# Kernel tuning notes

Hardware: AMD Instinct MI355X
Metric: run time of the kernel (lower is better)

## Reference

```python
import jax, jax.numpy as jnp
import numpy as np

B, T, TM = 4, 1024, 1500
D_MODEL, D_FFN, H, D_HEAD, D_MEM = 1024, 4096, 16, 64, 1024
EPS = 1e-5


def layernorm(x, g):
    m = jnp.mean(x, axis=-1, keepdims=True)
    xc = x - m
    v = jnp.mean(xc * xc, axis=-1, keepdims=True)
    return xc * jax.lax.rsqrt(v + EPS) * g


def setup_inputs() -> dict:
    key = jax.random.key(0)
    ks = jax.random.split(key, 12)
    s = lambda fan_in: 1.0 / np.sqrt(fan_in)
    return {
        "x": jax.random.normal(ks[0], (B, T, D_MODEL), jnp.float32),
        "encoder_output": jax.random.normal(ks[1], (B, TM, D_MEM), jnp.float32),
        "encoder_mask": jax.random.randint(ks[2], (B, TM), 0, 2).astype(bool),
        "w_qkv": jax.random.normal(ks[3], (D_MODEL, 3 * H * D_HEAD), jnp.float32) * s(D_MODEL),
        "w_o_sa": jax.random.normal(ks[4], (H * D_HEAD, D_MODEL), jnp.float32) * s(H * D_HEAD),
        "w_q": jax.random.normal(ks[5], (D_MODEL, H * D_HEAD), jnp.float32) * s(D_MODEL),
        "w_kv": jax.random.normal(ks[6], (D_MEM, 2 * H * D_HEAD), jnp.float32) * s(D_MEM),
        "w_o_xa": jax.random.normal(ks[7], (H * D_HEAD, D_MODEL), jnp.float32) * s(H * D_HEAD),
        "w_ff1": jax.random.normal(ks[8], (D_MODEL, D_FFN), jnp.float32) * s(D_MODEL),
        "w_ff2": jax.random.normal(ks[9], (D_FFN, D_MODEL), jnp.float32) * s(D_FFN),
        "g_sa": jnp.ones((D_MODEL,), jnp.float32),
        "g_xaq": jnp.ones((D_MODEL,), jnp.float32),
        "g_xam": jnp.ones((D_MEM,), jnp.float32),
        "g_ff": jnp.ones((D_MODEL,), jnp.float32),
    }


def reference(x, encoder_output, encoder_mask, w_qkv, w_o_sa, w_q, w_kv, w_o_xa,
              w_ff1, w_ff2, g_sa, g_xaq, g_xam, g_ff):
    b, t, _ = x.shape
    scale = D_HEAD ** -0.5

    # ---- causal self-attention ----
    residual = x
    xn = layernorm(x, g_sa)
    qkv = (xn @ w_qkv).reshape(b, t, 3, H, D_HEAD)
    q, k, v = qkv[:, :, 0], qkv[:, :, 1], qkv[:, :, 2]  # (B,T,H,D)
    scores = jnp.einsum('bqhd,bkhd->bhqk', q, k) * scale
    causal = jnp.tril(jnp.ones((t, t), x.dtype))
    scores = scores + (1.0 - causal) * -1e9
    attn = jax.nn.softmax(scores, axis=-1)
    sa = jnp.einsum('bhqk,bkhd->bqhd', attn, v).reshape(b, t, H * D_HEAD)
    x = residual + sa @ w_o_sa

    # ---- cross-attention ----
    residual = x
    qn = layernorm(x, g_xaq)
    mn = layernorm(encoder_output, g_xam)
    tq, tm = t, mn.shape[1]
    qx = (qn @ w_q).reshape(b, tq, H, D_HEAD)
    kvx = (mn @ w_kv).reshape(b, tm, 2, H, D_HEAD)
    kx, vx = kvx[:, :, 0], kvx[:, :, 1]
    xs = jnp.einsum('bqhd,bkhd->bhqk', qx, kx) * scale
    xs = jnp.where(encoder_mask[:, None, None, :], xs, -jnp.inf)
    xattn = jax.nn.softmax(xs, axis=-1)
    xa = jnp.einsum('bhqk,bkhd->bqhd', xattn, vx).reshape(b, tq, H * D_HEAD)
    x = residual + xa @ w_o_xa

    # ---- pointwise FFN (kernel_size=1 conv == linear) ----
    residual = x
    h = layernorm(x, g_ff)
    h = jax.nn.gelu(h @ w_ff1, approximate=True) @ w_ff2
    x = residual + h
    return (x, k, v)
```

## Files before the change

### kernel.cpp

```cpp
#include <hip/hip_runtime.h>
#include <hip/hip_bf16.h>
#include <cstdint>
#include <cstddef>


typedef __attribute__((ext_vector_type(4))) float f32x4;
typedef __attribute__((ext_vector_type(8))) short s8v;
typedef __attribute__((ext_vector_type(2))) unsigned uint2v;

#define DEVI __device__ __forceinline__

DEVI short f2bf(float f) {
  union { float f; unsigned u; } x; x.f = f;
  unsigned r = x.u + 0x7fffu + ((x.u >> 16) & 1u);
  return (short)(r >> 16);
}
DEVI float bf2f(short s) {
  union { unsigned u; float f; } x; x.u = ((unsigned)(unsigned short)s) << 16;
  return x.f;
}
DEVI unsigned cvtpk_bf2(float lo, float hi) {
  unsigned r;
  asm("v_cvt_pk_bf16_f32 %0, %1, %2" : "=v"(r) : "v"(lo), "v"(hi));
  return r;
}
DEVI float fexp2(float x) {
  float r;
  asm("v_exp_f32 %0, %1" : "=v"(r) : "v"(x));
  return r;
}
DEVI float bpermf(int srclane, float v) {
  union { float f; int i; } x; x.f = v;
  x.i = __builtin_amdgcn_ds_bpermute(srclane << 2, x.i);
  return x.f;
}
DEVI void gload_lds16(const void* g, void* l) {
  __builtin_amdgcn_global_load_lds((const __attribute__((address_space(1))) void*)g,
                                   (__attribute__((address_space(3))) void*)l,
                                   16, 0, 0);
}

__global__ __launch_bounds__(256) void k_transpose_cvt(
    const float* __restrict__ w, short* __restrict__ wt, int K, int N) {
  __shared__ float tile[32][33];
  int n0 = blockIdx.x * 32, k0 = blockIdx.y * 32;
  int tx = threadIdx.x & 31, ty = threadIdx.x >> 5;
#pragma unroll
  for (int i = 0; i < 32; i += 8)
    tile[ty + i][tx] = w[(size_t)(k0 + ty + i) * N + n0 + tx];
  __syncthreads();
#pragma unroll
  for (int i = 0; i < 32; i += 8)
    wt[(size_t)(n0 + ty + i) * K + k0 + tx] = f2bf(tile[tx][ty + i]);
}

__global__ __launch_bounds__(256) void k_vtrans(
    const short* __restrict__ src, int srs, int coff,
    short* __restrict__ dst, int T, int Tp) {
  __shared__ short tile[32][72];
  int bh = blockIdx.y, b = bh >> 4, h = bh & 15;
  int t0 = blockIdx.x * 32;
  const short* sB = src + (size_t)b * T * srs + coff + h * 64;
  short* dB = dst + (size_t)bh * 64 * Tp;
  int t = threadIdx.x;
  int r = t >> 3, c = (t & 7) * 8;
  int tr = t0 + r; if (tr > T - 1) tr = T - 1;
  *(s8v*)&tile[r][c] = *(const s8v*)(sB + (size_t)tr * srs + c);
  __syncthreads();
  int d = t & 63, ch = t >> 6;
  s8v o;
#pragma unroll
  for (int j = 0; j < 8; j++) o[j] = tile[ch * 8 + j][d];
  *(s8v*)(dB + (size_t)d * Tp + t0 + ch * 8) = o;
}

__global__ void k_maskpack(const int* __restrict__ mask,
                           unsigned long long* __restrict__ out, int Tk, int mw) {
  int b = blockIdx.x, w = threadIdx.x;
  if (w >= mw) return;
  unsigned long long v = 0;
  const int* mb = mask + (size_t)b * Tk;
#pragma unroll 4
  for (int j = 0; j < 64; j++) {
    int k = w * 64 + j;
    if (k < Tk && mb[k]) v |= (1ull << j);
  }
  out[(size_t)b * mw + w] = v;
}

__global__ __launch_bounds__(256) void k_ln(
    const float* __restrict__ x, const float* __restrict__ g,
    short* __restrict__ out) {
  int row = blockIdx.x;
  const float* xr = x + (size_t)row * 1024;
  int t = threadIdx.x, wid = t >> 6, lane = t & 63;
  f32x4 v = ((const f32x4*)xr)[t];
  float s = v[0] + v[1] + v[2] + v[3];
#pragma unroll
  for (int m = 32; m >= 1; m >>= 1) s += __shfl_xor(s, m);
  __shared__ float red[4];
  if (lane == 0) red[wid] = s;
  __syncthreads();
  float mean = (red[0] + red[1] + red[2] + red[3]) * (1.f / 1024.f);
  float q = 0.f;
#pragma unroll
  for (int i = 0; i < 4; i++) { v[i] -= mean; q += v[i] * v[i]; }
#pragma unroll
  for (int m = 32; m >= 1; m >>= 1) q += __shfl_xor(q, m);
  __syncthreads();
  if (lane == 0) red[wid] = q;
  __syncthreads();
  float var = (red[0] + red[1] + red[2] + red[3]) * (1.f / 1024.f);
  float rs = rsqrtf(var + 1e-5f);
  f32x4 gv = ((const f32x4*)g)[t];
  unsigned w0 = cvtpk_bf2(v[0] * rs * gv[0], v[1] * rs * gv[1]);
  unsigned w1 = cvtpk_bf2(v[2] * rs * gv[2], v[3] * rs * gv[3]);
  uint2v w = {w0, w1};
  *(uint2v*)(out + (size_t)row * 1024 + t * 4) = w;
}

template <bool RES, bool GELU_, bool F32OUT, bool BF16OUT>
__global__ __launch_bounds__(256) void k_gemm(
    const short* __restrict__ A, const short* __restrict__ Bt,
    float* __restrict__ Cf, short* __restrict__ Cb,
    const float* __restrict__ res, int M, int N, int K, int lda, int ldb) {
  __shared__ short As[128 * 64];
  __shared__ short Bs[128 * 64];
  int z = blockIdx.z;
  A += (size_t)z * K;
  Bt += (size_t)z * K;
  if (F32OUT) Cf += (size_t)z * M * N;
  int t = threadIdx.x, wid = t >> 6, lane = t & 63;
  int la = lane & 15, lb = lane >> 4;
  int wr = wid >> 1, wc = wid & 1;
  int am = blockIdx.x * 128, bn = blockIdx.y * 128;

  f32x4 acc[4][4];
#pragma unroll
  for (int m = 0; m < 4; m++)
#pragma unroll
    for (int n = 0; n < 4; n++) acc[m][n] = (f32x4){0.f, 0.f, 0.f, 0.f};

  for (int k0 = 0; k0 < K; k0 += 64) {
#pragma unroll
    for (int i = 0; i < 4; i++) {
      int fl = i * 256 + t;
      int r = fl >> 3;
      int c = ((fl & 7) ^ (r & 7)) << 3;
      int ar = am + r; if (ar > M - 1) ar = M - 1;
      gload_lds16(A + (size_t)ar * lda + k0 + c, As + (size_t)(i * 256 + wid * 64) * 8);
      int br = bn + r;
      gload_lds16(Bt + (size_t)br * ldb + k0 + c, Bs + (size_t)(i * 256 + wid * 64) * 8);
    }
    __syncthreads();
#pragma unroll
    for (int kk = 0; kk < 2; kk++) {
      s8v af[4], bfg[4];
#pragma unroll
      for (int m = 0; m < 4; m++)
        af[m] = *(const s8v*)(As + (wr * 64 + m * 16 + la) * 64 +
                              ((kk * 32 + lb * 8) ^ ((la & 7) << 3)));
#pragma unroll
      for (int n = 0; n < 4; n++)
        bfg[n] = *(const s8v*)(Bs + (wc * 64 + n * 16 + la) * 64 +
                               ((kk * 32 + lb * 8) ^ ((la & 7) << 3)));
#pragma unroll
      for (int m = 0; m < 4; m++)
#pragma unroll
        for (int n = 0; n < 4; n++)
          acc[m][n] = __builtin_amdgcn_mfma_f32_16x16x32_bf16(af[m], bfg[n], acc[m][n], 0, 0, 0);
    }
    __syncthreads();
  }

#pragma unroll
  for (int m = 0; m < 4; m++) {
    int rb = am + wr * 64 + m * 16 + lb * 4;
#pragma unroll
    for (int n = 0; n < 4; n++) {
      int col = bn + wc * 64 + n * 16 + la;
#pragma unroll
      for (int j = 0; j < 4; j++) {
        int r = rb + j;
        if (r < M) {
          float v = acc[m][n][j];
          if (RES) v += res[(size_t)r * N + col];
          if (GELU_) {
            float u = v;
            float y = 0.7978845608f * u * (1.f + 0.044715f * u * u);
            float e = fexp2(fminf(y * 2.88539008f, 80.f));
            float th = (e - 1.f) * __builtin_amdgcn_rcpf(e + 1.f);
            v = 0.5f * u * (1.f + th);
          }
          if (F32OUT) Cf[(size_t)r * N + col] = v;
          if (BF16OUT) Cb[(size_t)r * N + col] = f2bf(v);
        }
      }
    }
  }
}

__global__ __launch_bounds__(256) void k_red4(
    const f32x4* __restrict__ p, const f32x4* __restrict__ res,
    f32x4* __restrict__ out, int n) {
  size_t i = (size_t)blockIdx.x * 256 + threadIdx.x;
  f32x4 v = res[i] + (p[i] + p[i + (size_t)n]) +
            (p[i + 2 * (size_t)n] + p[i + 3 * (size_t)n]);
  out[i] = v;
}

template <bool CAUSAL>
__global__ __launch_bounds__(512) void k_attn4(
    const short* __restrict__ qbuf, int qrs,
    const short* __restrict__ kbuf, int krs,
    const short* __restrict__ vT, int vts,
    short* __restrict__ obuf, int ors,
    const unsigned long long* __restrict__ mbits, int mwords,
    int Tq, int Tk, float scale) {
  __shared__ short Ks[64 * 64];
  __shared__ short Vs[64 * 64];
  __shared__ short Ps[8 * 1024];
  int bh = blockIdx.y, b = bh >> 4, h = bh & 15;
  int t = threadIdx.x, wid = t >> 6, lane = t & 63;
  int la = lane & 15, lb = lane >> 4;
  float lscale = scale * 1.44269504f;

  const short* qB = qbuf + (size_t)b * Tq * qrs + h * 64;
  const short* kB = kbuf + (size_t)b * Tk * krs + h * 64;
  const short* vB = vT + (size_t)bh * 64 * vts;
  char* Pw = (char*)(Ps + wid * 1024);

  int sr = t >> 3, scol = (t & 7) * 8;
  int swz = sr * 64 + (scol ^ ((sr & 7) << 3));

  int nsup = CAUSAL ? 2 : 1;
  for (int s = 0; s < nsup; s++) {
    int st = CAUSAL ? (s ? 7 - blockIdx.x : blockIdx.x) : blockIdx.x;
    int q0 = st * 128 + wid * 16;
    int nkt = CAUSAL ? 2 * st + 2 : (Tk + 63) >> 6;
    int lastkt = CAUSAL ? (q0 >> 6) : nkt - 1;

    s8v qf[2];
#pragma unroll
    for (int kk = 0; kk < 2; kk++)
      qf[kk] = *(const s8v*)(qB + (size_t)(q0 + la) * qrs + kk * 32 + lb * 8);

    f32x4 accO[4];
#pragma unroll
    for (int n = 0; n < 4; n++) accO[n] = (f32x4){0.f, 0.f, 0.f, 0.f};
    float m = -1e30f, l = 0.f;

    s8v krg, vrg;
    {
      int tk = sr; if (tk > Tk - 1) tk = Tk - 1;
      krg = *(const s8v*)(kB + (size_t)tk * krs + scol);
      vrg = *(const s8v*)(vB + (size_t)sr * vts + scol);
    }

    for (int kt = 0; kt < nkt; kt++) {
      int kb0 = kt << 6;
      __syncthreads();
      *(s8v*)&Ks[swz] = krg;
      *(s8v*)&Vs[swz] = vrg;
      __syncthreads();
      if (kt + 1 < nkt) {
        int kb = kb0 + 64;
        int tk = kb + sr; if (tk > Tk - 1) tk = Tk - 1;
        krg = *(const s8v*)(kB + (size_t)tk * krs + scol);
        vrg = *(const s8v*)(vB + (size_t)sr * vts + kb + scol);
      }
      if (kt > lastkt) continue;

      bool needMask;
      unsigned long long wm = ~0ull;
      if (CAUSAL) {
        needMask = (kt == lastkt);
      } else {
        wm = mbits[(size_t)b * mwords + kt];
        needMask = (wm != ~0ull);
      }

      float sc[4][4];
      __builtin_amdgcn_s_setprio(1);
#pragma unroll
      for (int n = 0; n < 4; n++) {
        f32x4 a = (f32x4){0.f, 0.f, 0.f, 0.f};
#pragma unroll
        for (int kk = 0; kk < 2; kk++) {
          s8v kf = *(const s8v*)&Ks[(n * 16 + la) * 64 +
                                    ((kk * 32 + lb * 8) ^ ((la & 7) << 3))];
          a = __builtin_amdgcn_mfma_f32_16x16x32_bf16(kf, qf[kk], a, 0, 0, 0);
        }
#pragma unroll
        for (int j = 0; j < 4; j++) {
          float sv = a[j] * lscale;
          if (needMask) {
            int ki = n * 16 + lb * 4 + j;
            bool ok = CAUSAL ? (kb0 + ki <= q0 + la) : (((wm >> ki) & 1ull) != 0);
            sv = ok ? sv : -1e30f;
          }
          sc[n][j] = sv;
        }
      }
      __builtin_amdgcn_s_setprio(0);

      float tm = sc[0][0];
#pragma unroll
      for (int n = 0; n < 4; n++)
#pragma unroll
        for (int j = 0; j < 4; j++) tm = fmaxf(tm, sc[n][j]);
      tm = fmaxf(tm, __shfl_xor(tm, 16));
      tm = fmaxf(tm, __shfl_xor(tm, 32));
      tm = fmaxf(tm, -1e4f);

      bool skip = __all(tm - m <= 10.f);
      float alpha = 1.f;
      if (!skip) {
        float mn_ = fmaxf(m, tm);
        alpha = fexp2(m - mn_);
        m = mn_;
      }

      unsigned W[4][2];
      float ps = 0.f;
#pragma unroll
      for (int n = 0; n < 4; n++) {
        float p0 = fexp2(sc[n][0] - m), p1 = fexp2(sc[n][1] - m);
        float p2 = fexp2(sc[n][2] - m), p3 = fexp2(sc[n][3] - m);
        ps += (p0 + p1) + (p2 + p3);
        W[n][0] = cvtpk_bf2(p0, p1);
        W[n][1] = cvtpk_bf2(p2, p3);
      }
      ps += __shfl_xor(ps, 16);
      ps += __shfl_xor(ps, 32);
      l = l * alpha + ps;

      if (!skip) {
#pragma unroll
        for (int j = 0; j < 4; j++) {
          float aj = bpermf(lb * 20 + j, alpha);
#pragma unroll
          for (int n = 0; n < 4; n++) accO[n][j] *= aj;
        }
      }

#pragma unroll
      for (int n = 0; n < 4; n++) {
        uint2v w2 = {W[n][0], W[n][1]};
        *(uint2v*)(Pw + ((la * 128 + n * 32 + lb * 8) ^ ((la & 7) << 4))) = w2;
      }
      __builtin_amdgcn_s_setprio(1);
#pragma unroll
      for (int kk = 0; kk < 2; kk++) {
        s8v pa = *(const s8v*)(Pw + ((la * 128 + kk * 64 + lb * 16) ^ ((la & 7) << 4)));
#pragma unroll
        for (int n = 0; n < 4; n++) {
          s8v vf = *(const s8v*)&Vs[(n * 16 + la) * 64 +
                                    ((kk * 32 + lb * 8) ^ ((la & 7) << 3))];
          accO[n] = __builtin_amdgcn_mfma_f32_16x16x32_bf16(pa, vf, accO[n], 0, 0, 0);
        }
      }
      __builtin_amdgcn_s_setprio(0);
    }

#pragma unroll
    for (int j = 0; j < 4; j++) {
      float lj = bpermf(lb * 20 + j, l);
      float inv = 1.f / lj;
      int r = q0 + lb * 4 + j;
#pragma unroll
      for (int n = 0; n < 4; n++)
        obuf[(size_t)(b * Tq + r) * ors + h * 64 + n * 16 + la] = f2bf(accO[n][j] * inv);
    }
  }
}

__global__ __launch_bounds__(256) void k_copy_kv(
    const short* __restrict__ qkvb, float* __restrict__ ok, float* __restrict__ ov) {
  size_t i = (size_t)blockIdx.x * 256 + threadIdx.x;
  size_t row = i >> 7, c8 = (i & 127) << 3;
  const short* base = qkvb + row * 3072;
  s8v kv = *(const s8v*)(base + 1024 + c8);
  s8v vv = *(const s8v*)(base + 2048 + c8);
  f32x4 k0, k1, v0, v1;
#pragma unroll
  for (int j = 0; j < 4; j++) {
    k0[j] = bf2f(kv[j]); k1[j] = bf2f(kv[4 + j]);
    v0[j] = bf2f(vv[j]); v1[j] = bf2f(vv[4 + j]);
  }
  float* okp = ok + row * 1024 + c8;
  float* ovp = ov + row * 1024 + c8;
  *(f32x4*)okp = k0; *(f32x4*)(okp + 4) = k1;
  *(f32x4*)ovp = v0; *(f32x4*)(ovp + 4) = v1;
}

extern "C" void kernel_launch(void* const* d_in, const int* in_sizes, int n_in,
                              void* d_out, int out_size, void* d_ws, size_t ws_size,
                              hipStream_t stream) {
  (void)in_sizes; (void)n_in; (void)out_size; (void)ws_size;
  const float* x      = (const float*)d_in[0];
  const float* enc    = (const float*)d_in[1];
  const int*   mask   = (const int*)d_in[2];
  const float* w_qkv  = (const float*)d_in[3];
  const float* w_o_sa = (const float*)d_in[4];
  const float* w_q    = (const float*)d_in[5];
  const float* w_kv   = (const float*)d_in[6];
  const float* w_o_xa = (const float*)d_in[7];
  const float* w_ff1  = (const float*)d_in[8];
  const float* w_ff2  = (const float*)d_in[9];
  const float* g_sa   = (const float*)d_in[10];
  const float* g_xaq  = (const float*)d_in[11];
  const float* g_xam  = (const float*)d_in[12];
  const float* g_ff   = (const float*)d_in[13];

  float* out_x = (float*)d_out;
  float* out_k = out_x + (size_t)4096 * 1024;
  float* out_v = out_k + (size_t)4096 * 1024;

  char* ws = (char*)d_ws;
  size_t off = 0;
  auto alloc = [&](size_t bytes) -> void* {
    void* p = ws + off;
    off += (bytes + 255) & ~(size_t)255;
    return p;
  };
  short* wqkv_t = (short*)alloc((size_t)3072 * 1024 * 2);
  short* wosa_t = (short*)alloc((size_t)1024 * 1024 * 2);
  short* wq_t   = (short*)alloc((size_t)1024 * 1024 * 2);
  short* wkv_t  = (short*)alloc((size_t)2048 * 1024 * 2);
  short* woxa_t = (short*)alloc((size_t)1024 * 1024 * 2);
  short* wff1_t = (short*)alloc((size_t)4096 * 1024 * 2);
  short* wff2_t = (short*)alloc((size_t)1024 * 4096 * 2);
  short* xn     = (short*)alloc((size_t)4096 * 1024 * 2);
  short* qkv_b  = (short*)alloc((size_t)4096 * 3072 * 2);
  short* sa_b   = (short*)alloc((size_t)4096 * 1024 * 2);
  float* x1     = (float*)alloc((size_t)4096 * 1024 * 4);
  short* qn     = (short*)alloc((size_t)4096 * 1024 * 2);
  short* mn     = (short*)alloc((size_t)6000 * 1024 * 2);
  short* qx_b   = (short*)alloc((size_t)4096 * 1024 * 2);
  short* kvx_b  = (short*)alloc((size_t)6000 * 2048 * 2);
  short* xa_b   = (short*)alloc((size_t)4096 * 1024 * 2);
  float* x2     = (float*)alloc((size_t)4096 * 1024 * 4);
  short* hn     = (short*)alloc((size_t)4096 * 1024 * 2);
  short* h1     = (short*)alloc((size_t)4096 * 4096 * 2);
  unsigned long long* mbits = (unsigned long long*)alloc(4 * 24 * 8);

  short* vTsa = xn;
  short* vTxa = h1;
  float* part = (float*)qkv_b;

  k_transpose_cvt<<<dim3(96, 32), 256, 0, stream>>>(w_qkv, wqkv_t, 1024, 3072);
  k_transpose_cvt<<<dim3(32, 32), 256, 0, stream>>>(w_o_sa, wosa_t, 1024, 1024);
  k_transpose_cvt<<<dim3(32, 32), 256, 0, stream>>>(w_q, wq_t, 1024, 1024);
  k_transpose_cvt<<<dim3(64, 32), 256, 0, stream>>>(w_kv, wkv_t, 1024, 2048);
  k_transpose_cvt<<<dim3(32, 32), 256, 0, stream>>>(w_o_xa, woxa_t, 1024, 1024);
  k_transpose_cvt<<<dim3(128, 32), 256, 0, stream>>>(w_ff1, wff1_t, 1024, 4096);
  k_transpose_cvt<<<dim3(32, 128), 256, 0, stream>>>(w_ff2, wff2_t, 4096, 1024);
  k_maskpack<<<4, 64, 0, stream>>>(mask, mbits, 1500, 24);

  k_ln<<<4096, 256, 0, stream>>>(x, g_sa, xn);
  k_gemm<false, false, false, true><<<dim3(32, 24), 256, 0, stream>>>(
      xn, wqkv_t, nullptr, qkv_b, nullptr, 4096, 3072, 1024, 1024, 1024);
  k_copy_kv<<<2048, 256, 0, stream>>>(qkv_b, out_k, out_v);
  k_vtrans<<<dim3(32, 64), 256, 0, stream>>>(qkv_b, 3072, 2048, vTsa, 1024, 1024);
  k_attn4<true><<<dim3(4, 64), 512, 0, stream>>>(
      qkv_b, 3072, qkv_b + 1024, 3072, vTsa, 1024,
      sa_b, 1024, nullptr, 0, 1024, 1024, 0.125f);
  k_gemm<true, false, true, false><<<dim3(32, 8), 256, 0, stream>>>(
      sa_b, wosa_t, x1, nullptr, x, 4096, 1024, 1024, 1024, 1024);

  k_ln<<<4096, 256, 0, stream>>>(x1, g_xaq, qn);
  k_ln<<<6000, 256, 0, stream>>>(enc, g_xam, mn);
  k_gemm<false, false, false, true><<<dim3(32, 8), 256, 0, stream>>>(
      qn, wq_t, nullptr, qx_b, nullptr, 4096, 1024, 1024, 1024, 1024);
  k_gemm<false, false, false, true><<<dim3(47, 16), 256, 0, stream>>>(
      mn, wkv_t, nullptr, kvx_b, nullptr, 6000, 2048, 1024, 1024, 1024);
  k_vtrans<<<dim3(48, 64), 256, 0, stream>>>(kvx_b, 2048, 1024, vTxa, 1500, 1536);
  k_attn4<false><<<dim3(8, 64), 512, 0, stream>>>(
      qx_b, 1024, kvx_b, 2048, vTxa, 1536,
      xa_b, 1024, mbits, 24, 1024, 1500, 0.125f);
  k_gemm<true, false, true, false><<<dim3(32, 8), 256, 0, stream>>>(
      xa_b, woxa_t, x2, nullptr, x1, 4096, 1024, 1024, 1024, 1024);

  k_ln<<<4096, 256, 0, stream>>>(x2, g_ff, hn);
  k_gemm<false, true, false, true><<<dim3(32, 32), 256, 0, stream>>>(
      hn, wff1_t, nullptr, h1, nullptr, 4096, 4096, 1024, 1024, 1024);
  k_gemm<false, false, true, false><<<dim3(32, 8, 4), 256, 0, stream>>>(
      h1, wff2_t, part, nullptr, nullptr, 4096, 1024, 1024, 4096, 4096);
  k_red4<<<4096, 256, 0, stream>>>(
      (const f32x4*)part, (const f32x4*)x2, (f32x4*)out_x, 1048576);
}
```

Baseline: 455.8 us.

## Double-buffer GEMM LDS, swizzle block order, fuse K/V output, halve FFN2 split-K

```diff
diff --git a/kernel.cpp b/kernel.cpp
--- a/kernel.cpp
+++ b/kernel.cpp
@@ -119,21 +119,31 @@
   *(uint2v*)(out + (size_t)row * 1024 + t * 4) = w;
 }
 
-template <bool RES, bool GELU_, bool F32OUT, bool BF16OUT>
+template <bool RES, bool GELU_, bool F32OUT, bool BF16OUT, bool KV>
 __global__ __launch_bounds__(256) void k_gemm(
     const short* __restrict__ A, const short* __restrict__ Bt,
     float* __restrict__ Cf, short* __restrict__ Cb,
-    const float* __restrict__ res, int M, int N, int K, int lda, int ldb) {
-  __shared__ short As[128 * 64];
-  __shared__ short Bs[128 * 64];
+    const float* __restrict__ res, float* __restrict__ okv,
+    int M, int N, int K, int lda, int ldb) {
+  __shared__ short As0[128 * 64];
+  __shared__ short Bs0[128 * 64];
+  __shared__ short As1[128 * 64];
+  __shared__ short Bs1[128 * 64];
   int z = blockIdx.z;
   A += (size_t)z * K;
   Bt += (size_t)z * K;
   if (F32OUT) Cf += (size_t)z * M * N;
+
+  int nxy = gridDim.x * gridDim.y;
+  int orig = blockIdx.y * gridDim.x + blockIdx.x;
+  int cpx = nxy >> 3;
+  int swzb = (orig & 7) * cpx + (orig >> 3);
+  int bx = swzb % gridDim.x, by = swzb / gridDim.x;
+
   int t = threadIdx.x, wid = t >> 6, lane = t & 63;
   int la = lane & 15, lb = lane >> 4;
   int wr = wid >> 1, wc = wid & 1;
-  int am = blockIdx.x * 128, bn = blockIdx.y * 128;
+  int am = bx * 128, bn = by * 128;
 
   f32x4 acc[4][4];
 #pragma unroll
@@ -141,28 +151,28 @@
 #pragma unroll
     for (int n = 0; n < 4; n++) acc[m][n] = (f32x4){0.f, 0.f, 0.f, 0.f};
 
-  for (int k0 = 0; k0 < K; k0 += 64) {
+  auto STAGE = [&](short* Asb, short* Bsb, int k0) {
 #pragma unroll
     for (int i = 0; i < 4; i++) {
       int fl = i * 256 + t;
       int r = fl >> 3;
       int c = ((fl & 7) ^ (r & 7)) << 3;
       int ar = am + r; if (ar > M - 1) ar = M - 1;
-      gload_lds16(A + (size_t)ar * lda + k0 + c, As + (size_t)(i * 256 + wid * 64) * 8);
-      int br = bn + r;
-      gload_lds16(Bt + (size_t)br * ldb + k0 + c, Bs + (size_t)(i * 256 + wid * 64) * 8);
-    }
-    __syncthreads();
+      gload_lds16(A + (size_t)ar * lda + k0 + c, Asb + (size_t)(i * 256 + wid * 64) * 8);
+      gload_lds16(Bt + (size_t)(bn + r) * ldb + k0 + c, Bsb + (size_t)(i * 256 + wid * 64) * 8);
+    }
+  };
+  auto COMP = [&](const short* Asb, const short* Bsb) {
 #pragma unroll
     for (int kk = 0; kk < 2; kk++) {
       s8v af[4], bfg[4];
 #pragma unroll
       for (int m = 0; m < 4; m++)
-        af[m] = *(const s8v*)(As + (wr * 64 + m * 16 + la) * 64 +
+        af[m] = *(const s8v*)(Asb + (wr * 64 + m * 16 + la) * 64 +
                               ((kk * 32 + lb * 8) ^ ((la & 7) << 3)));
 #pragma unroll
       for (int n = 0; n < 4; n++)
-        bfg[n] = *(const s8v*)(Bs + (wc * 64 + n * 16 + la) * 64 +
+        bfg[n] = *(const s8v*)(Bsb + (wc * 64 + n * 16 + la) * 64 +
                                ((kk * 32 + lb * 8) ^ ((la & 7) << 3)));
 #pragma unroll
       for (int m = 0; m < 4; m++)
@@ -170,6 +180,17 @@
         for (int n = 0; n < 4; n++)
           acc[m][n] = __builtin_amdgcn_mfma_f32_16x16x32_bf16(af[m], bfg[n], acc[m][n], 0, 0, 0);
     }
+  };
+
+  STAGE(As0, Bs0, 0);
+  __syncthreads();
+  int nk = K >> 6;
+  for (int kb = 0; kb < nk; kb += 2) {
+    STAGE(As1, Bs1, (kb + 1) << 6);
+    COMP(As0, Bs0);
+    __syncthreads();
+    if (kb + 2 < nk) STAGE(As0, Bs0, (kb + 2) << 6);
+    COMP(As1, Bs1);
     __syncthreads();
   }
 
@@ -194,19 +215,23 @@
           }
           if (F32OUT) Cf[(size_t)r * N + col] = v;
           if (BF16OUT) Cb[(size_t)r * N + col] = f2bf(v);
+          if (KV) {
+            if (col >= 2048)
+              okv[(size_t)4096 * 1024 + (size_t)r * 1024 + (col - 2048)] = v;
+            else if (col >= 1024)
+              okv[(size_t)r * 1024 + (col - 1024)] = v;
+          }
         }
       }
     }
   }
 }
 
-__global__ __launch_bounds__(256) void k_red4(
+__global__ __launch_bounds__(256) void k_red2(
     const f32x4* __restrict__ p, const f32x4* __restrict__ res,
     f32x4* __restrict__ out, int n) {
   size_t i = (size_t)blockIdx.x * 256 + threadIdx.x;
-  f32x4 v = res[i] + (p[i] + p[i + (size_t)n]) +
-            (p[i + 2 * (size_t)n] + p[i + 3 * (size_t)n]);
-  out[i] = v;
+  out[i] = res[i] + (p[i] + p[i + (size_t)n]);
 }
 
 template <bool CAUSAL>
@@ -373,25 +398,6 @@
         obuf[(size_t)(b * Tq + r) * ors + h * 64 + n * 16 + la] = f2bf(accO[n][j] * inv);
     }
   }
-}
-
-__global__ __launch_bounds__(256) void k_copy_kv(
-    const short* __restrict__ qkvb, float* __restrict__ ok, float* __restrict__ ov) {
-  size_t i = (size_t)blockIdx.x * 256 + threadIdx.x;
-  size_t row = i >> 7, c8 = (i & 127) << 3;
-  const short* base = qkvb + row * 3072;
-  s8v kv = *(const s8v*)(base + 1024 + c8);
-  s8v vv = *(const s8v*)(base + 2048 + c8);
-  f32x4 k0, k1, v0, v1;
-#pragma unroll
-  for (int j = 0; j < 4; j++) {
-    k0[j] = bf2f(kv[j]); k1[j] = bf2f(kv[4 + j]);
-    v0[j] = bf2f(vv[j]); v1[j] = bf2f(vv[4 + j]);
-  }
-  float* okp = ok + row * 1024 + c8;
-  float* ovp = ov + row * 1024 + c8;
-  *(f32x4*)okp = k0; *(f32x4*)(okp + 4) = k1;
-  *(f32x4*)ovp = v0; *(f32x4*)(ovp + 4) = v1;
 }
 
 extern "C" void kernel_launch(void* const* d_in, const int* in_sizes, int n_in,
@@ -415,7 +421,6 @@
 
   float* out_x = (float*)d_out;
   float* out_k = out_x + (size_t)4096 * 1024;
-  float* out_v = out_k + (size_t)4096 * 1024;
 
   char* ws = (char*)d_ws;
   size_t off = 0;
@@ -459,34 +464,33 @@
   k_maskpack<<<4, 64, 0, stream>>>(mask, mbits, 1500, 24);
 
   k_ln<<<4096, 256, 0, stream>>>(x, g_sa, xn);
-  k_gemm<false, false, false, true><<<dim3(32, 24), 256, 0, stream>>>(
-      xn, wqkv_t, nullptr, qkv_b, nullptr, 4096, 3072, 1024, 1024, 1024);
-  k_copy_kv<<<2048, 256, 0, stream>>>(qkv_b, out_k, out_v);
+  k_gemm<false, false, false, true, true><<<dim3(32, 24), 256, 0, stream>>>(
+      xn, wqkv_t, nullptr, qkv_b, nullptr, out_k, 4096, 3072, 1024, 1024, 1024);
   k_vtrans<<<dim3(32, 64), 256, 0, stream>>>(qkv_b, 3072, 2048, vTsa, 1024, 1024);
   k_attn4<true><<<dim3(4, 64), 512, 0, stream>>>(
       qkv_b, 3072, qkv_b + 1024, 3072, vTsa, 1024,
       sa_b, 1024, nullptr, 0, 1024, 1024, 0.125f);
-  k_gemm<true, false, true, false><<<dim3(32, 8), 256, 0, stream>>>(
-      sa_b, wosa_t, x1, nullptr, x, 4096, 1024, 1024, 1024, 1024);
+  k_gemm<true, false, true, false, false><<<dim3(32, 8), 256, 0, stream>>>(
+      sa_b, wosa_t, x1, nullptr, x, nullptr, 4096, 1024, 1024, 1024, 1024);
 
   k_ln<<<4096, 256, 0, stream>>>(x1, g_xaq, qn);
   k_ln<<<6000, 256, 0, stream>>>(enc, g_xam, mn);
-  k_gemm<false, false, false, true><<<dim3(32, 8), 256, 0, stream>>>(
-      qn, wq_t, nullptr, qx_b, nullptr, 4096, 1024, 1024, 1024, 1024);
-  k_gemm<false, false, false, true><<<dim3(47, 16), 256, 0, stream>>>(
-      mn, wkv_t, nullptr, kvx_b, nullptr, 6000, 2048, 1024, 1024, 1024);
+  k_gemm<false, false, false, true, false><<<dim3(32, 8), 256, 0, stream>>>(
+      qn, wq_t, nullptr, qx_b, nullptr, nullptr, 4096, 1024, 1024, 1024, 1024);
+  k_gemm<false, false, false, true, false><<<dim3(47, 16), 256, 0, stream>>>(
+      mn, wkv_t, nullptr, kvx_b, nullptr, nullptr, 6000, 2048, 1024, 1024, 1024);
   k_vtrans<<<dim3(48, 64), 256, 0, stream>>>(kvx_b, 2048, 1024, vTxa, 1500, 1536);
   k_attn4<false><<<dim3(8, 64), 512, 0, stream>>>(
       qx_b, 1024, kvx_b, 2048, vTxa, 1536,
       xa_b, 1024, mbits, 24, 1024, 1500, 0.125f);
-  k_gemm<true, false, true, false><<<dim3(32, 8), 256, 0, stream>>>(
-      xa_b, woxa_t, x2, nullptr, x1, 4096, 1024, 1024, 1024, 1024);
+  k_gemm<true, false, true, false, false><<<dim3(32, 8), 256, 0, stream>>>(
+      xa_b, woxa_t, x2, nullptr, x1, nullptr, 4096, 1024, 1024, 1024, 1024);
 
   k_ln<<<4096, 256, 0, stream>>>(x2, g_ff, hn);
-  k_gemm<false, true, false, true><<<dim3(32, 32), 256, 0, stream>>>(
-      hn, wff1_t, nullptr, h1, nullptr, 4096, 4096, 1024, 1024, 1024);
-  k_gemm<false, false, true, false><<<dim3(32, 8, 4), 256, 0, stream>>>(
-      h1, wff2_t, part, nullptr, nullptr, 4096, 1024, 1024, 4096, 4096);
-  k_red4<<<4096, 256, 0, stream>>>(
+  k_gemm<false, true, false, true, false><<<dim3(32, 32), 256, 0, stream>>>(
+      hn, wff1_t, nullptr, h1, nullptr, nullptr, 4096, 4096, 1024, 1024, 1024);
+  k_gemm<false, false, true, false, false><<<dim3(32, 8, 2), 256, 0, stream>>>(
+      h1, wff2_t, part, nullptr, nullptr, nullptr, 4096, 1024, 2048, 4096, 4096);
+  k_red2<<<4096, 256, 0, stream>>>(
       (const f32x4*)part, (const f32x4*)x2, (f32x4*)out_x, 1048576);
 }
```

Result: no change. 452.9 us (-0.6%).
